# Performance work log

Measured on AMD Instinct MI355X. Metric: run time of the kernel, lower is better.

## Reference

```python
import jax, jax.numpy as jnp
import numpy as np
from functools import partial

ALPHA = 0.99   # EMA smoothing factor of unbiasedExponentialSmoother
EPS = 1e-5

def setup_inputs() -> dict:
    key = jax.random.key(0)
    B, C, T = 8, 256, 16384
    x = jax.random.normal(key, (B, C, T), dtype=jnp.float32)
    return {"x": x}

def _causal_unbiased_ema_norm(x, alpha, eps):
    # x: [B, C, T]. Causal instance norm: per (b, c) lane, running unbiased
    # EMA estimates of mean and second moment over time, then normalize.
    B, C, T = x.shape
    xt = jnp.transpose(x, (2, 0, 1))  # [T, B, C] time-major for scan

    def step(carry, xi):
        s1, s2, w = carry
        s1 = alpha * s1 + (1.0 - alpha) * xi          # EMA of x
        s2 = alpha * s2 + (1.0 - alpha) * xi * xi     # EMA of x^2
        w = alpha * w + (1.0 - alpha)                 # bias correction 1-alpha^t
        mean = s1 / w
        var = s2 / w - mean * mean
        out = (xi - mean) * jax.lax.rsqrt(var + eps)
        return (s1, s2, w), out

    z = jnp.zeros((B, C), dtype=x.dtype)
    w0 = jnp.zeros((), dtype=x.dtype)
    _, yt = jax.lax.scan(step, (z, z, w0), xt)
    return jnp.transpose(yt, (1, 2, 0))  # back to [B, C, T]

def reference(x):
    # MyInstanceNorm1d(causal=True, use_unbiasEMA=True, affine=False):
    # permute/unsqueeze wrapper around the causal unbiased-EMA smoother.
    return _causal_unbiased_ema_norm(x, ALPHA, EPS)
```

## Files before the change

### kernel.cpp

```cpp
#include <hip/hip_runtime.h>

#define T_LEN  16384
#define CHUNK  64
#define NTHR   256

__global__ __launch_bounds__(NTHR, 2)
void ema_norm_kernel(const float* __restrict__ x, float* __restrict__ y) {
    const float A    = 0.99f;
    const float OMA  = (float)(1.0 - 0.99);
    const float EPSF = 1e-5f;
    const float Kf = (float)((double)((float)(1.0 - 0.99)) / (1.0 - (double)0.99f));

    const int row  = blockIdx.x;
    const int tid  = threadIdx.x;
    const int lane = tid & 63;
    const int wid  = tid >> 6;

    const float4* __restrict__ xr =
        reinterpret_cast<const float4*>(x + (size_t)row * T_LEN + (size_t)tid * CHUNK);
    float4* __restrict__ yr =
        reinterpret_cast<float4*>(y + (size_t)row * T_LEN + (size_t)tid * CHUNK);

    float4 xv[16];
#pragma unroll
    for (int i = 0; i < 16; ++i) xv[i] = xr[i];

    float s1 = 0.f, s2 = 0.f;
#pragma unroll
    for (int i = 0; i < 16; ++i) {
        float t;
        t = OMA * xv[i].x; s1 = fmaf(A, s1, t); s2 = fmaf(A, s2, t * xv[i].x);
        t = OMA * xv[i].y; s1 = fmaf(A, s1, t); s2 = fmaf(A, s2, t * xv[i].y);
        t = OMA * xv[i].z; s1 = fmaf(A, s1, t); s2 = fmaf(A, s2, t * xv[i].z);
        t = OMA * xv[i].w; s1 = fmaf(A, s1, t); s2 = fmaf(A, s2, t * xv[i].w);
    }

    float a64 = A;
#pragma unroll
    for (int i = 0; i < 6; ++i) a64 *= a64;
    float d[8];
    d[0] = a64;
#pragma unroll
    for (int k = 1; k < 8; ++k) d[k] = d[k - 1] * d[k - 1];

    float v1 = s1, v2 = s2;
#pragma unroll
    for (int k = 0; k < 6; ++k) {
        const int off = 1 << k;
        float o1 = __shfl_up(v1, off, 64);
        float o2 = __shfl_up(v2, off, 64);
        if (lane >= off) { v1 = fmaf(d[k], o1, v1); v2 = fmaf(d[k], o2, v2); }
    }
    float c1 = __shfl_up(v1, 1, 64);
    float c2 = __shfl_up(v2, 1, 64);
    if (lane == 0) { c1 = 0.f; c2 = 0.f; }

    __shared__ float tot1[4], tot2[4];
    if (lane == 63) { tot1[wid] = v1; tot2[wid] = v2; }
    __syncthreads();
    float W1 = 0.f, W2 = 0.f;
    const float Dw = d[6];
    for (int v = 0; v < wid; ++v) {
        W1 = fmaf(W1, Dw, tot1[v]);
        W2 = fmaf(W2, Dw, tot2[v]);
    }
    float fdec = 1.f;
#pragma unroll
    for (int k = 0; k < 6; ++k) if (lane & (1 << k)) fdec *= d[k];
    c1 = fmaf(W1, fdec, c1);
    c2 = fmaf(W2, fdec, c2);

    float pw = 1.f;
#pragma unroll
    for (int k = 0; k < 8; ++k) if (tid & (1 << k)) pw *= d[k];
    float wrun = (tid == 0) ? 0.f : Kf * (1.f - pw);

    s1 = c1; s2 = c2;
#pragma unroll
    for (int i = 0; i < 16; ++i) {
        float4 xq = xv[i];
        float4 oq;
        {   float xi = xq.x; float t = OMA * xi;
            s1 = fmaf(A, s1, t); s2 = fmaf(A, s2, t * xi);
            wrun = fmaf(A, wrun, OMA);
            float invw = 1.0f / wrun;
            float mean = s1 * invw;
            float var  = fmaf(-mean, mean, s2 * invw);
            float rs   = __builtin_amdgcn_rsqf(var + EPSF);
            oq.x = (xi - mean) * rs; }
        {   float xi = xq.y; float t = OMA * xi;
            s1 = fmaf(A, s1, t); s2 = fmaf(A, s2, t * xi);
            wrun = fmaf(A, wrun, OMA);
            float invw = 1.0f / wrun;
            float mean = s1 * invw;
            float var  = fmaf(-mean, mean, s2 * invw);
            float rs   = __builtin_amdgcn_rsqf(var + EPSF);
            oq.y = (xi - mean) * rs; }
        {   float xi = xq.z; float t = OMA * xi;
            s1 = fmaf(A, s1, t); s2 = fmaf(A, s2, t * xi);
            wrun = fmaf(A, wrun, OMA);
            float invw = 1.0f / wrun;
            float mean = s1 * invw;
            float var  = fmaf(-mean, mean, s2 * invw);
            float rs   = __builtin_amdgcn_rsqf(var + EPSF);
            oq.z = (xi - mean) * rs; }
        {   float xi = xq.w; float t = OMA * xi;
            s1 = fmaf(A, s1, t); s2 = fmaf(A, s2, t * xi);
            wrun = fmaf(A, wrun, OMA);
            float invw = 1.0f / wrun;
            float mean = s1 * invw;
            float var  = fmaf(-mean, mean, s2 * invw);
            float rs   = __builtin_amdgcn_rsqf(var + EPSF);
            oq.w = (xi - mean) * rs; }
        yr[i] = oq;
    }
}

extern "C" void kernel_launch(void* const* d_in, const int* in_sizes, int n_in,
                              void* d_out, int out_size, void* d_ws, size_t ws_size,
                              hipStream_t stream) {
    const float* x = (const float*)d_in[0];
    float* y = (float*)d_out;
    const int rows = in_sizes[0] / T_LEN;
    ema_norm_kernel<<<rows, NTHR, 0, stream>>>(x, y);
}
```

Measured before the change: 287.1 us.

## Stage row chunks through LDS for coalesced loads and stores with prefetch

The row is now processed in four 4096-element chunks. Each chunk is loaded with coalesced float4 accesses, transposed through padded shared memory so each thread gets 16 contiguous elements, and the next chunk is prefetched into registers. A running carry across chunks replaces the single whole-row scan, and results go back through LDS so the global stores are coalesced too. It also removes the per-element division by computing (x*w - s1) * rsq(s2*w - s1^2 + eps*w^2) and raises the occupancy hint, at the cost of extra barriers and LDS traffic.

After: 236.3 us. 1.21x faster.

```diff
diff --git a/kernel.cpp b/kernel.cpp
--- a/kernel.cpp
+++ b/kernel.cpp
@@ -1,119 +1,130 @@
 #include <hip/hip_runtime.h>
 
-#define T_LEN  16384
-#define CHUNK  64
 #define NTHR   256
+#define NWAVE  4
+#define CH4    1024
+#define ROW4   4096
+#define PAD4(i) ((i) + ((i) >> 4))
 
-__global__ __launch_bounds__(NTHR, 2)
+
+constexpr float fsq(float v) { return v * v; }
+constexpr float A_    = 0.99f;
+constexpr float OMA_  = (float)(1.0 - 0.99);
+constexpr float D16   = fsq(fsq(fsq(fsq(A_))));
+constexpr float D32   = fsq(D16);
+constexpr float D64   = fsq(D32);
+constexpr float D128  = fsq(D64);
+constexpr float D256  = fsq(D128);
+constexpr float D512  = fsq(D256);
+constexpr float D1K   = fsq(D512);
+constexpr float D2K   = fsq(D1K);
+constexpr float D4K   = fsq(D2K);
+constexpr float D8K   = fsq(D4K);
+constexpr float D12K  = D4K * D8K;
+constexpr float KF    = (float)((double)OMA_ / (1.0 - (double)A_));
+
+__device__ __forceinline__ float4 norm4(float4 xq, float& s1, float& s2, float& w) {
+    constexpr float EPSF = 1e-5f;
+    float4 oq;
+    { float xi = xq.x; float t = OMA_*xi; s1 = fmaf(A_,s1,t); s2 = fmaf(A_,s2,t*xi);
+      w = fmaf(A_,w,OMA_);
+      float nu = fmaf(xi,w,-s1); float ag = fmaf(s2,w,fmaf(-s1,s1,EPSF*(w*w)));
+      oq.x = nu * __builtin_amdgcn_rsqf(ag); }
+    { float xi = xq.y; float t = OMA_*xi; s1 = fmaf(A_,s1,t); s2 = fmaf(A_,s2,t*xi);
+      w = fmaf(A_,w,OMA_);
+      float nu = fmaf(xi,w,-s1); float ag = fmaf(s2,w,fmaf(-s1,s1,EPSF*(w*w)));
+      oq.y = nu * __builtin_amdgcn_rsqf(ag); }
+    { float xi = xq.z; float t = OMA_*xi; s1 = fmaf(A_,s1,t); s2 = fmaf(A_,s2,t*xi);
+      w = fmaf(A_,w,OMA_);
+      float nu = fmaf(xi,w,-s1); float ag = fmaf(s2,w,fmaf(-s1,s1,EPSF*(w*w)));
+      oq.z = nu * __builtin_amdgcn_rsqf(ag); }
+    { float xi = xq.w; float t = OMA_*xi; s1 = fmaf(A_,s1,t); s2 = fmaf(A_,s2,t*xi);
+      w = fmaf(A_,w,OMA_);
+      float nu = fmaf(xi,w,-s1); float ag = fmaf(s2,w,fmaf(-s1,s1,EPSF*(w*w)));
+      oq.w = nu * __builtin_amdgcn_rsqf(ag); }
+    return oq;
+}
+
+#define ACC4(q) { float t; \
+    t = OMA_*(q).x; s1 = fmaf(A_,s1,t); s2 = fmaf(A_,s2,t*(q).x); \
+    t = OMA_*(q).y; s1 = fmaf(A_,s1,t); s2 = fmaf(A_,s2,t*(q).y); \
+    t = OMA_*(q).z; s1 = fmaf(A_,s1,t); s2 = fmaf(A_,s2,t*(q).z); \
+    t = OMA_*(q).w; s1 = fmaf(A_,s1,t); s2 = fmaf(A_,s2,t*(q).w); }
+
+#define WS(OFF, DK) { float o1 = __shfl_up(v1, OFF, 64), o2 = __shfl_up(v2, OFF, 64); \
+    if (lane >= OFF) { v1 = fmaf(DK, o1, v1); v2 = fmaf(DK, o2, v2); } }
+
+#define EMA_ITER(IT, CA,CB,CC,CD, NA,NB,NC,ND, PREF, PWIT) do { \
+    if (PREF) { const float4* p = xr4 + (IT+1)*CH4 + tid; \
+        NA = p[0]; NB = p[256]; NC = p[512]; ND = p[768]; } \
+    buf[PAD4(tid)]     = CA; buf[PAD4(tid+256)] = CB; \
+    buf[PAD4(tid+512)] = CC; buf[PAD4(tid+768)] = CD; \
+    __syncthreads(); \
+    float4 x0 = buf[PAD4(4*tid)],   x1 = buf[PAD4(4*tid+1)]; \
+    float4 x2 = buf[PAD4(4*tid+2)], x3 = buf[PAD4(4*tid+3)]; \
+    float s1 = 0.f, s2 = 0.f; \
+    ACC4(x0); ACC4(x1); ACC4(x2); ACC4(x3); \
+    float v1 = s1, v2 = s2; \
+    WS(1, D16) WS(2, D32) WS(4, D64) WS(8, D128) WS(16, D256) WS(32, D512) \
+    float e1 = __shfl_up(v1, 1, 64), e2 = __shfl_up(v2, 1, 64); \
+    if (lane == 0) { e1 = 0.f; e2 = 0.f; } \
+    if (lane == 63) { tW1[wid] = v1; tW2[wid] = v2; } \
+    __syncthreads(); \
+    float W1 = C1, W2 = C2, myW1 = C1, myW2 = C2; \
+    if (wid == 0) { myW1 = W1; myW2 = W2; } \
+    W1 = fmaf(D1K, W1, tW1[0]); W2 = fmaf(D1K, W2, tW2[0]); \
+    if (wid == 1) { myW1 = W1; myW2 = W2; } \
+    W1 = fmaf(D1K, W1, tW1[1]); W2 = fmaf(D1K, W2, tW2[1]); \
+    if (wid == 2) { myW1 = W1; myW2 = W2; } \
+    W1 = fmaf(D1K, W1, tW1[2]); W2 = fmaf(D1K, W2, tW2[2]); \
+    if (wid == 3) { myW1 = W1; myW2 = W2; } \
+    W1 = fmaf(D1K, W1, tW1[3]); W2 = fmaf(D1K, W2, tW2[3]); \
+    C1 = W1; C2 = W2; \
+    float cc1 = fmaf(myW1, fdec, e1), cc2 = fmaf(myW2, fdec, e2); \
+    float ww = KF * (1.f - pwtid * (PWIT)); \
+    x0 = norm4(x0, cc1, cc2, ww); x1 = norm4(x1, cc1, cc2, ww); \
+    x2 = norm4(x2, cc1, cc2, ww); x3 = norm4(x3, cc1, cc2, ww); \
+    buf[PAD4(4*tid)]   = x0; buf[PAD4(4*tid+1)] = x1; \
+    buf[PAD4(4*tid+2)] = x2; buf[PAD4(4*tid+3)] = x3; \
+    __syncthreads(); \
+    float4* q = yr4 + (IT)*CH4 + tid; \
+    q[0] = buf[PAD4(tid)];     q[256] = buf[PAD4(tid+256)]; \
+    q[512] = buf[PAD4(tid+512)]; q[768] = buf[PAD4(tid+768)]; \
+    __syncthreads(); \
+} while (0)
+
+__global__ __launch_bounds__(NTHR, 4)
 void ema_norm_kernel(const float* __restrict__ x, float* __restrict__ y) {
-    const float A    = 0.99f;
-    const float OMA  = (float)(1.0 - 0.99);
-    const float EPSF = 1e-5f;
-    const float Kf = (float)((double)((float)(1.0 - 0.99)) / (1.0 - (double)0.99f));
-
-    const int row  = blockIdx.x;
     const int tid  = threadIdx.x;
     const int lane = tid & 63;
     const int wid  = tid >> 6;
 
-    const float4* __restrict__ xr =
-        reinterpret_cast<const float4*>(x + (size_t)row * T_LEN + (size_t)tid * CHUNK);
-    float4* __restrict__ yr =
-        reinterpret_cast<float4*>(y + (size_t)row * T_LEN + (size_t)tid * CHUNK);
+    const float4* __restrict__ xr4 = reinterpret_cast<const float4*>(x) + (size_t)blockIdx.x * ROW4;
+    float4*       __restrict__ yr4 = reinterpret_cast<float4*>(y) + (size_t)blockIdx.x * ROW4;
 
-    float4 xv[16];
-#pragma unroll
-    for (int i = 0; i < 16; ++i) xv[i] = xr[i];
+    __shared__ float4 buf[CH4 + CH4 / 16];
+    __shared__ float  tW1[NWAVE], tW2[NWAVE];
 
-    float s1 = 0.f, s2 = 0.f;
-#pragma unroll
-    for (int i = 0; i < 16; ++i) {
-        float t;
-        t = OMA * xv[i].x; s1 = fmaf(A, s1, t); s2 = fmaf(A, s2, t * xv[i].x);
-        t = OMA * xv[i].y; s1 = fmaf(A, s1, t); s2 = fmaf(A, s2, t * xv[i].y);
-        t = OMA * xv[i].z; s1 = fmaf(A, s1, t); s2 = fmaf(A, s2, t * xv[i].z);
-        t = OMA * xv[i].w; s1 = fmaf(A, s1, t); s2 = fmaf(A, s2, t * xv[i].w);
-    }
+    float fdec = 1.f;
+    if (lane & 1)  fdec *= D16;
+    if (lane & 2)  fdec *= D32;
+    if (lane & 4)  fdec *= D64;
+    if (lane & 8)  fdec *= D128;
+    if (lane & 16) fdec *= D256;
+    if (lane & 32) fdec *= D512;
+    float pwtid = fdec;
+    if (tid & 64)  pwtid *= D1K;
+    if (tid & 128) pwtid *= D2K;
 
-    float a64 = A;
-#pragma unroll
-    for (int i = 0; i < 6; ++i) a64 *= a64;
-    float d[8];
-    d[0] = a64;
-#pragma unroll
-    for (int k = 1; k < 8; ++k) d[k] = d[k - 1] * d[k - 1];
+    float C1 = 0.f, C2 = 0.f;
 
-    float v1 = s1, v2 = s2;
-#pragma unroll
-    for (int k = 0; k < 6; ++k) {
-        const int off = 1 << k;
-        float o1 = __shfl_up(v1, off, 64);
-        float o2 = __shfl_up(v2, off, 64);
-        if (lane >= off) { v1 = fmaf(d[k], o1, v1); v2 = fmaf(d[k], o2, v2); }
-    }
-    float c1 = __shfl_up(v1, 1, 64);
-    float c2 = __shfl_up(v2, 1, 64);
-    if (lane == 0) { c1 = 0.f; c2 = 0.f; }
+    float4 a0, a1, a2, a3, b0, b1, b2, b3;
+    { const float4* p = xr4 + tid; a0 = p[0]; a1 = p[256]; a2 = p[512]; a3 = p[768]; }
 
-    __shared__ float tot1[4], tot2[4];
-    if (lane == 63) { tot1[wid] = v1; tot2[wid] = v2; }
-    __syncthreads();
-    float W1 = 0.f, W2 = 0.f;
-    const float Dw = d[6];
-    for (int v = 0; v < wid; ++v) {
-        W1 = fmaf(W1, Dw, tot1[v]);
-        W2 = fmaf(W2, Dw, tot2[v]);
-    }
-    float fdec = 1.f;
-#pragma unroll
-    for (int k = 0; k < 6; ++k) if (lane & (1 << k)) fdec *= d[k];
-    c1 = fmaf(W1, fdec, c1);
-    c2 = fmaf(W2, fdec, c2);
-
-    float pw = 1.f;
-#pragma unroll
-    for (int k = 0; k < 8; ++k) if (tid & (1 << k)) pw *= d[k];
-    float wrun = (tid == 0) ? 0.f : Kf * (1.f - pw);
-
-    s1 = c1; s2 = c2;
-#pragma unroll
-    for (int i = 0; i < 16; ++i) {
-        float4 xq = xv[i];
-        float4 oq;
-        {   float xi = xq.x; float t = OMA * xi;
-            s1 = fmaf(A, s1, t); s2 = fmaf(A, s2, t * xi);
-            wrun = fmaf(A, wrun, OMA);
-            float invw = 1.0f / wrun;
-            float mean = s1 * invw;
-            float var  = fmaf(-mean, mean, s2 * invw);
-            float rs   = __builtin_amdgcn_rsqf(var + EPSF);
-            oq.x = (xi - mean) * rs; }
-        {   float xi = xq.y; float t = OMA * xi;
-            s1 = fmaf(A, s1, t); s2 = fmaf(A, s2, t * xi);
-            wrun = fmaf(A, wrun, OMA);
-            float invw = 1.0f / wrun;
-            float mean = s1 * invw;
-            float var  = fmaf(-mean, mean, s2 * invw);
-            float rs   = __builtin_amdgcn_rsqf(var + EPSF);
-            oq.y = (xi - mean) * rs; }
-        {   float xi = xq.z; float t = OMA * xi;
-            s1 = fmaf(A, s1, t); s2 = fmaf(A, s2, t * xi);
-            wrun = fmaf(A, wrun, OMA);
-            float invw = 1.0f / wrun;
-            float mean = s1 * invw;
-            float var  = fmaf(-mean, mean, s2 * invw);
-            float rs   = __builtin_amdgcn_rsqf(var + EPSF);
-            oq.z = (xi - mean) * rs; }
-        {   float xi = xq.w; float t = OMA * xi;
-            s1 = fmaf(A, s1, t); s2 = fmaf(A, s2, t * xi);
-            wrun = fmaf(A, wrun, OMA);
-            float invw = 1.0f / wrun;
-            float mean = s1 * invw;
-            float var  = fmaf(-mean, mean, s2 * invw);
-            float rs   = __builtin_amdgcn_rsqf(var + EPSF);
-            oq.w = (xi - mean) * rs; }
-        yr[i] = oq;
-    }
+    EMA_ITER(0, a0,a1,a2,a3, b0,b1,b2,b3, true,  1.0f);
+    EMA_ITER(1, b0,b1,b2,b3, a0,a1,a2,a3, true,  D4K);
+    EMA_ITER(2, a0,a1,a2,a3, b0,b1,b2,b3, true,  D8K);
+    EMA_ITER(3, b0,b1,b2,b3, a0,a1,a2,a3, false, D12K);
 }
 
 extern "C" void kernel_launch(void* const* d_in, const int* in_sizes, int n_in,
@@ -121,6 +132,6 @@
                               hipStream_t stream) {
     const float* x = (const float*)d_in[0];
     float* y = (float*)d_out;
-    const int rows = in_sizes[0] / T_LEN;
+    const int rows = in_sizes[0] / 16384;
     ema_norm_kernel<<<rows, NTHR, 0, stream>>>(x, y);
 }
```
